# Optimization experiments

Hardware: AMD Instinct MI355X
Metric: run time of the kernel (lower is better)

The kernel has to match this reference:

```python
import math
import jax, jax.numpy as jnp
import numpy as np


def setup_inputs() -> dict:
    key = jax.random.key(0)
    ks = jax.random.split(key, 6)
    b, k, t, h = 4, 128, 2048, 8
    s = 0.05
    return {
        "x": jax.random.normal(ks[0], (b, k, t), dtype=jnp.float32),
        "Wq": jax.random.normal(ks[1], (h * k, k), dtype=jnp.float32) * s,
        "Wk": jax.random.normal(ks[2], (h * k, k), dtype=jnp.float32) * s,
        "Wv": jax.random.normal(ks[3], (h * k, k), dtype=jnp.float32) * s,
        "Wu": jax.random.normal(ks[4], (k, h * k), dtype=jnp.float32) * s,
        "bu": jax.random.normal(ks[5], (k,), dtype=jnp.float32) * s,
    }


def reference(x, Wq, Wk, Wv, Wu, bu):
    b, k, t = x.shape
    h = Wq.shape[0] // k

    def proj(W):
        # x: [b,k,t], W: [h*k, k] -> [b,h,k,t]
        return jnp.einsum('bkt,jk->bjt', x, W).reshape(b, h, k, t)

    q = proj(Wq)
    keys = proj(Wk)
    v = proj(Wv)

    # scores: [b,h,t,t], scaled by 1/sqrt(k)
    dot = jnp.einsum('bhkt,bhki->bhti', q, keys) / math.sqrt(k)
    attn = jax.nn.softmax(dot, axis=-1)

    # attend: [b,h,k,t]
    o = jnp.einsum('bhti,bhki->bhkt', attn, v)

    # unify heads: Wu [k, h*k] viewed as [k,h,k]
    Wu3 = Wu.reshape(k, h, k)
    out = jnp.einsum('bhet,khe->bkt', o, Wu3)
    return out + bu[None, :, None]
```

## Files before the change

kernel.cpp:

```cpp
#include <hip/hip_runtime.h>
#include <hip/hip_bf16.h>

using short8 = __attribute__((ext_vector_type(8))) short;
using f32x4  = __attribute__((ext_vector_type(4))) float;
using f32x16 = __attribute__((ext_vector_type(16))) float;
using uint2v = __attribute__((ext_vector_type(2))) unsigned;

#define B_  4
#define KD  128
#define T_  2048
#define H_  8
#define HK  (H_*KD)
#define NT  (T_/64)

__device__ __forceinline__ ushort f2bf(float f) {
    unsigned u = __builtin_bit_cast(unsigned, f);
    u += 0x7fffu + ((u >> 16) & 1u);
    return (ushort)(u >> 16);
}

__device__ __forceinline__ unsigned cvt_pk_bf16(float lo, float hi) {
    unsigned r;
    asm("v_cvt_pk_bf16_f32 %0, %1, %2" : "=v"(r) : "v"(lo), "v"(hi));
    return r;
}

__global__ __launch_bounds__(256) void prep_kernel(const float* __restrict__ x,
                                                   const float* __restrict__ Wq,
                                                   const float* __restrict__ Wk,
                                                   const float* __restrict__ Wv,
                                                   const float* __restrict__ Wu,
                                                   ushort* __restrict__ wdst,
                                                   ushort* __restrict__ xt) {
    __shared__ float tile[64][65];
    int bx = blockIdx.x;
    if (bx < 2048) {
        int i = bx * 256 + threadIdx.x;
        const int n1 = HK * KD;
        const float* src = (i < n1) ? Wq : (i < 2*n1) ? Wk : (i < 3*n1) ? Wv : Wu;
        wdst[i] = f2bf(src[i & (n1 - 1)]);
        return;
    }
    int bi = bx - 2048;
    int t0 = (bi & 31) * 64;
    int k0 = ((bi >> 5) & 1) * 64;
    int b  = bi >> 6;
    int c  = threadIdx.x & 63;
    int r4 = threadIdx.x >> 6;
    #pragma unroll
    for (int i = 0; i < 16; i++) {
        int k = r4 * 16 + i;
        tile[k][c] = x[((size_t)b * KD + k0 + k) * T_ + t0 + c];
    }
    __syncthreads();
    #pragma unroll
    for (int i = 0; i < 16; i++) {
        int t = r4 * 16 + i;
        xt[((size_t)b * T_ + t0 + t) * KD + k0 + c] = f2bf(tile[c][t]);
    }
}

__global__ __launch_bounds__(256, 2) void proj_kernel(const ushort* __restrict__ xt,
                                                      const ushort* __restrict__ wall,
                                                      ushort* __restrict__ qtb,
                                                      ushort* __restrict__ ktb,
                                                      ushort* __restrict__ vsb) {
    int bz = blockIdx.y;
    int which = bz >> 2, b = bz & 3;
    int tidb = blockIdx.x;
    const ushort *A, *Bp;
    ushort* C;
    int N, m0, n0;
    float scale = 1.f;
    if (which < 2) {
        m0 = (tidb >> 3) * 128;
        n0 = (tidb & 7) * 128;
        A  = xt + (size_t)b * T_ * KD;
        Bp = wall + (size_t)which * (HK * KD);
        C  = (which ? ktb : qtb) + (size_t)b * T_ * HK;
        N  = HK;
        if (which == 0) scale = 0.08838834764831845f;
    } else {
        m0 = (tidb >> 4) * 128;
        n0 = (tidb & 15) * 128;
        A  = wall + (size_t)2 * (HK * KD);
        Bp = xt + (size_t)b * T_ * KD;
        C  = vsb + (size_t)b * HK * T_;
        N  = T_;
    }
    int lane = threadIdx.x & 63;
    int w    = threadIdx.x >> 6;
    int lq = lane & 31, hi = lane >> 5, hi8 = hi * 8;
    m0 += (w >> 1) * 64;
    n0 += (w & 1) * 64;

    const ushort* a0p = A  + (size_t)(m0 + lq) * KD + hi8;
    const ushort* a1p = A  + (size_t)(m0 + 32 + lq) * KD + hi8;
    const ushort* b0p = Bp + (size_t)(n0 + lq) * KD + hi8;
    const ushort* b1p = Bp + (size_t)(n0 + 32 + lq) * KD + hi8;

    short8 a0[8], a1[8], b0[8], b1[8];
    #pragma unroll
    for (int kc = 0; kc < 8; kc++) {
        a0[kc] = *(const short8*)(a0p + kc * 16);
        a1[kc] = *(const short8*)(a1p + kc * 16);
        b0[kc] = *(const short8*)(b0p + kc * 16);
        b1[kc] = *(const short8*)(b1p + kc * 16);
    }
    f32x16 acc[2][2] = {};
    #pragma unroll
    for (int kc = 0; kc < 8; kc++) {
        acc[0][0] = __builtin_amdgcn_mfma_f32_32x32x16_bf16(a0[kc], b0[kc], acc[0][0], 0, 0, 0);
        acc[0][1] = __builtin_amdgcn_mfma_f32_32x32x16_bf16(a0[kc], b1[kc], acc[0][1], 0, 0, 0);
        acc[1][0] = __builtin_amdgcn_mfma_f32_32x32x16_bf16(a1[kc], b0[kc], acc[1][0], 0, 0, 0);
        acc[1][1] = __builtin_amdgcn_mfma_f32_32x32x16_bf16(a1[kc], b1[kc], acc[1][1], 0, 0, 0);
    }
    #pragma unroll
    for (int i = 0; i < 2; i++)
        #pragma unroll
        for (int j = 0; j < 2; j++)
            #pragma unroll
            for (int r = 0; r < 16; r++) {
                int m = m0 + i*32 + (r & 3) + 8 * (r >> 2) + 4 * hi;
                int n = n0 + j*32 + lq;
                C[(size_t)m * N + n] = f2bf(acc[i][j][r] * scale);
            }
}

__global__ __launch_bounds__(256) void gemm_abT_f32bias(const ushort* __restrict__ A,
                                                        const ushort* __restrict__ B, long sB,
                                                        const float* __restrict__ bias,
                                                        float* __restrict__ C, long sC,
                                                        int M, int N, int Kd) {
    int b = blockIdx.z;
    B += (long)b * sB;  C += (long)b * sC;
    int lane = threadIdx.x & 63;
    int w    = threadIdx.x >> 6;
    int lr = lane & 15, lg = lane >> 4;
    int m0 = blockIdx.x * 64 + (w >> 1) * 32;
    int n0 = blockIdx.y * 64 + (w & 1) * 32;

    f32x4 acc[2][2] = {};
    #pragma unroll 4
    for (int k0 = 0; k0 < Kd; k0 += 32) {
        short8 af[2], bf[2];
        #pragma unroll
        for (int i = 0; i < 2; i++)
            af[i] = *(const short8*)(A + (long)(m0 + i*16 + lr) * Kd + k0 + lg*8);
        #pragma unroll
        for (int j = 0; j < 2; j++)
            bf[j] = *(const short8*)(B + (long)(n0 + j*16 + lr) * Kd + k0 + lg*8);
        #pragma unroll
        for (int i = 0; i < 2; i++)
            #pragma unroll
            for (int j = 0; j < 2; j++)
                acc[i][j] = __builtin_amdgcn_mfma_f32_16x16x32_bf16(af[i], bf[j], acc[i][j], 0, 0, 0);
    }
    #pragma unroll
    for (int i = 0; i < 2; i++)
        #pragma unroll
        for (int j = 0; j < 2; j++)
            #pragma unroll
            for (int r = 0; r < 4; r++) {
                int m = m0 + i*16 + lg*4 + r;
                int n = n0 + j*16 + lr;
                C[(long)m * N + n] = acc[i][j][r] + bias[m];
            }
}

__global__ __launch_bounds__(512, 2) void attn32_kernel(const ushort* __restrict__ qt,
                                                        const ushort* __restrict__ kt,
                                                        const ushort* __restrict__ vs,
                                                        ushort* __restrict__ ot) {
    int f = blockIdx.x;
    int xcd = f & 7, u = f >> 3;
    int qt8 = u & 7, gh = u >> 3;
    int g = xcd + 8 * gh;
    int h = g & 7, b = g >> 3;
    int w    = threadIdx.x >> 6;
    int lane = threadIdx.x & 63;
    int lq = lane & 31, hi = lane >> 5;
    int hi8 = hi * 8;
    int q0w = qt8 * 256 + w * 32;

    __shared__ __align__(16) ushort k_lds[2][64 * 128];
    __shared__ __align__(16) ushort v_lds[2][128 * 64];

    int tid  = threadIdx.x;
    int krow = tid >> 3, kcol = (tid & 7) << 4;
    const ushort* kst = kt + ((size_t)b * T_ + krow) * HK + h * KD + kcol;
    int kwi = krow * 128 + (kcol ^ ((krow & 7) << 3));
    int vrow = tid >> 2, vcol = (tid & 3) << 4;
    const ushort* vst = vs + ((size_t)b * HK + h * KD + vrow) * T_ + vcol;
    int vwi = vrow * 64 + (vcol ^ ((vrow & 7) << 3));

    const ushort* qbase = qt + ((size_t)b * T_ + q0w + lq) * HK + h * KD + hi8;

    short8 qf[8];
    #pragma unroll
    for (int dc = 0; dc < 8; dc++)
        qf[dc] = *(const short8*)(qbase + dc * 16);

    short8 rk0 = *(const short8*)(kst);
    short8 rk1 = *(const short8*)(kst + 8);
    short8 rv0 = *(const short8*)(vst);
    short8 rv1 = *(const short8*)(vst + 8);
    *(short8*)&k_lds[0][kwi]     = rk0;
    *(short8*)&k_lds[0][kwi ^ 8] = rk1;
    *(short8*)&v_lds[0][vwi]     = rv0;
    *(short8*)&v_lds[0][vwi ^ 8] = rv1;
    rk0 = *(const short8*)(kst + (size_t)64 * HK);
    rk1 = *(const short8*)(kst + (size_t)64 * HK + 8);
    rv0 = *(const short8*)(vst + 64);
    rv1 = *(const short8*)(vst + 64 + 8);
    __syncthreads();

    f32x16 o_acc[4] = {};
    float m_q = -1e30f, l_q = 0.f;
    const int xsw = (lq & 7) << 3;

    for (int t = 0; t < NT; ++t) {
        const int cur = t & 1;
        f32x16 s0 = {}, s1 = {};
        const ushort* kr0 = &k_lds[cur][(size_t)lq * 128];
        const ushort* kr1 = &k_lds[cur][(size_t)(32 + lq) * 128];
        #pragma unroll
        for (int dc = 0; dc < 8; dc++) {
            int c = (dc * 16 + hi8) ^ xsw;
            short8 kf0 = *(const short8*)(kr0 + c);
            short8 kf1 = *(const short8*)(kr1 + c);
            s0 = __builtin_amdgcn_mfma_f32_32x32x16_bf16(kf0, qf[dc], s0, 0, 0, 0);
            s1 = __builtin_amdgcn_mfma_f32_32x32x16_bf16(kf1, qf[dc], s1, 0, 0, 0);
        }

        float mx[8];
        #pragma unroll
        for (int i = 0; i < 8; i++)
            mx[i] = fmaxf(fmaxf(s0[i], s0[i+8]), fmaxf(s1[i], s1[i+8]));
        #pragma unroll
        for (int st = 4; st > 0; st >>= 1)
            #pragma unroll
            for (int i = 0; i < st; i++) mx[i] = fmaxf(mx[i], mx[i+st]);
        float pmax = fmaxf(mx[0], __shfl_xor(mx[0], 32));

        if (!__all(pmax - m_q <= 8.f)) {
            float mnew = fmaxf(m_q, pmax);
            float corr = __expf(m_q - mnew);
            l_q *= corr;
            m_q = mnew;
            #pragma unroll
            for (int r = 0; r < 16; r++) {
                float cr = __shfl(corr, (r & 3) + 8 * (r >> 2) + 4 * hi);
                #pragma unroll
                for (int dn = 0; dn < 4; dn++) o_acc[dn][r] *= cr;
            }
        }

        float ls0 = 0.f, ls1 = 0.f, ls2 = 0.f, ls3 = 0.f;
        #pragma unroll
        for (int r = 0; r < 16; r++) {
            float e0 = __expf(s0[r] - m_q);
            float e1 = __expf(s1[r] - m_q);
            s0[r] = e0; s1[r] = e1;
            if (r & 1) { ls1 += e0; ls3 += e1; } else { ls0 += e0; ls2 += e1; }
        }
        float lsum = (ls0 + ls1) + (ls2 + ls3);
        lsum += __shfl_xor(lsum, 32);
        l_q += lsum;

        unsigned uu[2][4][2];
        #pragma unroll
        for (int m4 = 0; m4 < 4; m4++) {
            uu[0][m4][0] = cvt_pk_bf16(s0[4*m4+0], s0[4*m4+1]);
            uu[0][m4][1] = cvt_pk_bf16(s0[4*m4+2], s0[4*m4+3]);
            uu[1][m4][0] = cvt_pk_bf16(s1[4*m4+0], s1[4*m4+1]);
            uu[1][m4][1] = cvt_pk_bf16(s1[4*m4+2], s1[4*m4+3]);
        }
        short8 ap[4];
        #pragma unroll
        for (int ks = 0; ks < 4; ks++) {
            int nt = ks >> 1, j = ks & 1;
            unsigned lo0 = uu[nt][2*j][0],   lo1 = uu[nt][2*j][1];
            unsigned hi0 = uu[nt][2*j+1][0], hi1 = uu[nt][2*j+1][1];
            uint2v r0 = __builtin_amdgcn_permlane32_swap(lo0, hi0, false, false);
            uint2v r1 = __builtin_amdgcn_permlane32_swap(lo1, hi1, false, false);
            union { unsigned wd[4]; short8 v; } c;
            c.wd[0] = r0[0];
            c.wd[1] = r1[0];
            c.wd[2] = r0[1];
            c.wd[3] = r1[1];
            ap[ks] = c.v;
        }

        #pragma unroll
        for (int dn = 0; dn < 4; dn++) {
            const ushort* vr = &v_lds[cur][(size_t)(dn*32 + lq) * 64];
            #pragma unroll
            for (int ks = 0; ks < 4; ks++) {
                int c = (ks * 16 + hi8) ^ xsw;
                short8 vf = *(const short8*)(vr + c);
                o_acc[dn] = __builtin_amdgcn_mfma_f32_32x32x16_bf16(ap[ks], vf, o_acc[dn], 0, 0, 0);
            }
        }

        __syncthreads();
        if (t + 1 < NT) {
            const int nxt = cur ^ 1;
            *(short8*)&k_lds[nxt][kwi]     = rk0;
            *(short8*)&k_lds[nxt][kwi ^ 8] = rk1;
            *(short8*)&v_lds[nxt][vwi]     = rv0;
            *(short8*)&v_lds[nxt][vwi ^ 8] = rv1;
            if (t + 2 < NT) {
                size_t ko = (size_t)(t + 2) * 64 * HK;
                int    vo = (t + 2) * 64;
                rk0 = *(const short8*)(kst + ko);
                rk1 = *(const short8*)(kst + ko + 8);
                rv0 = *(const short8*)(vst + vo);
                rv1 = *(const short8*)(vst + vo + 8);
            }
            __syncthreads();
        }
    }

    float linv = 1.f / l_q;
    ushort* ob = ot + ((size_t)b * T_ + q0w) * HK + h * KD;
    #pragma unroll
    for (int r = 0; r < 16; r++) {
        int qrow = (r & 3) + 8 * (r >> 2) + 4 * hi;
        float lr_ = __shfl(linv, qrow);
        #pragma unroll
        for (int dn = 0; dn < 4; dn++)
            ob[(size_t)qrow * HK + dn*32 + lq] = f2bf(o_acc[dn][r] * lr_);
    }
}

extern "C" void kernel_launch(void* const* d_in, const int* in_sizes, int n_in,
                              void* d_out, int out_size, void* d_ws, size_t ws_size,
                              hipStream_t stream) {
    const float* x  = (const float*)d_in[0];
    const float* Wq = (const float*)d_in[1];
    const float* Wk = (const float*)d_in[2];
    const float* Wv = (const float*)d_in[3];
    const float* Wu = (const float*)d_in[4];
    const float* bu = (const float*)d_in[5];
    float* out = (float*)d_out;

    const size_t XT  = (size_t)B_ * T_ * KD * 2;
    const size_t WB  = (size_t)HK * KD * 2;
    const size_t BIG = (size_t)B_ * T_ * HK * 2;
    size_t need = XT + 4*WB + 4*BIG;
    if (ws_size < need) return;

    char* p = (char*)d_ws;
    ushort* xt  = (ushort*)p;            p += XT;
    ushort* wqb = (ushort*)p;            p += WB;
    ushort* wkb = (ushort*)p;            p += WB;
    ushort* wvb = (ushort*)p;            p += WB;
    ushort* wub = (ushort*)p;            p += WB;
    ushort* qtb = (ushort*)p;            p += BIG;
    ushort* ktb = (ushort*)p;            p += BIG;
    ushort* vsb = (ushort*)p;            p += BIG;
    ushort* otb = (ushort*)p;            p += BIG;
    (void)wkb; (void)wvb;

    prep_kernel<<<2304, 256, 0, stream>>>(x, Wq, Wk, Wv, Wu, wqb, xt);

    proj_kernel<<<dim3(128, 12), 256, 0, stream>>>(xt, wqb, qtb, ktb, vsb);

    attn32_kernel<<<dim3(256), 512, 0, stream>>>(qtb, ktb, vsb, otb);

    gemm_abT_f32bias<<<dim3(KD/64, T_/64, B_), 256, 0, stream>>>(
        wub, otb, (long)T_*HK, bu, out, (long)KD*T_, KD, T_, HK);
}
```

Before: 129.7 us.

## Use FP8 for V and probabilities in attention PV matmul

Stores the V projection as FP8 (e4m3) and converts softmax probabilities to FP8, so the PV product runs on the fp8 32x32x16 MFMA and V global and LDS traffic is halved. The V LDS tile is re-laid out with a padded row stride and a new XOR swizzle. The online-softmax rescale threshold is also lowered from 8 to 5, which keeps unnormalized probabilities small enough for the FP8 range but triggers rescales more often. This cuts precision of P and V and risks accuracy loss. The V stores in the projection kernel become scattered byte writes.

```diff
diff --git a/kernel.cpp b/kernel.cpp
--- a/kernel.cpp
+++ b/kernel.cpp
@@ -12,6 +12,7 @@
 #define H_  8
 #define HK  (H_*KD)
 #define NT  (T_/64)
+#define VROW 72
 
 __device__ __forceinline__ ushort f2bf(float f) {
     unsigned u = __builtin_bit_cast(unsigned, f);
@@ -22,6 +23,17 @@
 __device__ __forceinline__ unsigned cvt_pk_bf16(float lo, float hi) {
     unsigned r;
     asm("v_cvt_pk_bf16_f32 %0, %1, %2" : "=v"(r) : "v"(lo), "v"(hi));
+    return r;
+}
+
+__device__ __forceinline__ unsigned cvt_pk_fp8_lo(unsigned old, float a, float b) {
+    unsigned r = old;
+    asm("v_cvt_pk_fp8_f32 %0, %1, %2" : "+v"(r) : "v"(a), "v"(b));
+    return r;
+}
+__device__ __forceinline__ unsigned cvt_pk_fp8_hi(unsigned old, float a, float b) {
+    unsigned r = old;
+    asm("v_cvt_pk_fp8_f32 %0, %1, %2 op_sel:[0,0,1]" : "+v"(r) : "v"(a), "v"(b));
     return r;
 }
 
@@ -64,12 +76,12 @@
                                                       const ushort* __restrict__ wall,
                                                       ushort* __restrict__ qtb,
                                                       ushort* __restrict__ ktb,
-                                                      ushort* __restrict__ vsb) {
+                                                      unsigned char* __restrict__ vsb) {
     int bz = blockIdx.y;
     int which = bz >> 2, b = bz & 3;
     int tidb = blockIdx.x;
     const ushort *A, *Bp;
-    ushort* C;
+    void* Cv;
     int N, m0, n0;
     float scale = 1.f;
     if (which < 2) {
@@ -77,7 +89,7 @@
         n0 = (tidb & 7) * 128;
         A  = xt + (size_t)b * T_ * KD;
         Bp = wall + (size_t)which * (HK * KD);
-        C  = (which ? ktb : qtb) + (size_t)b * T_ * HK;
+        Cv = (which ? ktb : qtb) + (size_t)b * T_ * HK;
         N  = HK;
         if (which == 0) scale = 0.08838834764831845f;
     } else {
@@ -85,7 +97,7 @@
         n0 = (tidb & 15) * 128;
         A  = wall + (size_t)2 * (HK * KD);
         Bp = xt + (size_t)b * T_ * KD;
-        C  = vsb + (size_t)b * HK * T_;
+        Cv = vsb + (size_t)b * HK * T_;
         N  = T_;
     }
     int lane = threadIdx.x & 63;
@@ -115,16 +127,32 @@
         acc[1][0] = __builtin_amdgcn_mfma_f32_32x32x16_bf16(a1[kc], b0[kc], acc[1][0], 0, 0, 0);
         acc[1][1] = __builtin_amdgcn_mfma_f32_32x32x16_bf16(a1[kc], b1[kc], acc[1][1], 0, 0, 0);
     }
-    #pragma unroll
-    for (int i = 0; i < 2; i++)
-        #pragma unroll
-        for (int j = 0; j < 2; j++)
-            #pragma unroll
-            for (int r = 0; r < 16; r++) {
-                int m = m0 + i*32 + (r & 3) + 8 * (r >> 2) + 4 * hi;
-                int n = n0 + j*32 + lq;
-                C[(size_t)m * N + n] = f2bf(acc[i][j][r] * scale);
-            }
+    if (which < 2) {
+        ushort* C = (ushort*)Cv;
+        #pragma unroll
+        for (int i = 0; i < 2; i++)
+            #pragma unroll
+            for (int j = 0; j < 2; j++)
+                #pragma unroll
+                for (int r = 0; r < 16; r++) {
+                    int m = m0 + i*32 + (r & 3) + 8 * (r >> 2) + 4 * hi;
+                    int n = n0 + j*32 + lq;
+                    C[(size_t)m * N + n] = f2bf(acc[i][j][r] * scale);
+                }
+    } else {
+        unsigned char* C = (unsigned char*)Cv;
+        #pragma unroll
+        for (int i = 0; i < 2; i++)
+            #pragma unroll
+            for (int j = 0; j < 2; j++)
+                #pragma unroll
+                for (int r = 0; r < 16; r++) {
+                    int m = m0 + i*32 + (r & 3) + 8 * (r >> 2) + 4 * hi;
+                    int n = n0 + j*32 + lq;
+                    float v = acc[i][j][r];
+                    C[(size_t)m * N + n] = (unsigned char)(cvt_pk_fp8_lo(0u, v, v) & 0xffu);
+                }
+    }
 }
 
 __global__ __launch_bounds__(256) void gemm_abT_f32bias(const ushort* __restrict__ A,
@@ -170,7 +198,7 @@
 
 __global__ __launch_bounds__(512, 2) void attn32_kernel(const ushort* __restrict__ qt,
                                                         const ushort* __restrict__ kt,
-                                                        const ushort* __restrict__ vs,
+                                                        const unsigned char* __restrict__ vs,
                                                         ushort* __restrict__ ot) {
     int f = blockIdx.x;
     int xcd = f & 7, u = f >> 3;
@@ -184,15 +212,15 @@
     int q0w = qt8 * 256 + w * 32;
 
     __shared__ __align__(16) ushort k_lds[2][64 * 128];
-    __shared__ __align__(16) ushort v_lds[2][128 * 64];
+    __shared__ __align__(16) unsigned char v_lds[2][128 * VROW];
 
     int tid  = threadIdx.x;
     int krow = tid >> 3, kcol = (tid & 7) << 4;
     const ushort* kst = kt + ((size_t)b * T_ + krow) * HK + h * KD + kcol;
     int kwi = krow * 128 + (kcol ^ ((krow & 7) << 3));
-    int vrow = tid >> 2, vcol = (tid & 3) << 4;
-    const ushort* vst = vs + ((size_t)b * HK + h * KD + vrow) * T_ + vcol;
-    int vwi = vrow * 64 + (vcol ^ ((vrow & 7) << 3));
+    int vrow = tid >> 2, vc16 = (tid & 3) << 4;
+    const unsigned char* vst = vs + ((size_t)b * HK + h * KD + vrow) * T_ + vc16;
+    int vwb = vrow * VROW + ((((vc16 >> 4) ^ (vrow & 3))) << 4);
 
     const ushort* qbase = qt + ((size_t)b * T_ + q0w + lq) * HK + h * KD + hi8;
 
@@ -203,21 +231,22 @@
 
     short8 rk0 = *(const short8*)(kst);
     short8 rk1 = *(const short8*)(kst + 8);
-    short8 rv0 = *(const short8*)(vst);
-    short8 rv1 = *(const short8*)(vst + 8);
+    long rvlo = *(const long*)(vst);
+    long rvhi = *(const long*)(vst + 8);
     *(short8*)&k_lds[0][kwi]     = rk0;
     *(short8*)&k_lds[0][kwi ^ 8] = rk1;
-    *(short8*)&v_lds[0][vwi]     = rv0;
-    *(short8*)&v_lds[0][vwi ^ 8] = rv1;
+    *(long*)&v_lds[0][vwb]       = rvlo;
+    *(long*)&v_lds[0][vwb + 8]   = rvhi;
     rk0 = *(const short8*)(kst + (size_t)64 * HK);
     rk1 = *(const short8*)(kst + (size_t)64 * HK + 8);
-    rv0 = *(const short8*)(vst + 64);
-    rv1 = *(const short8*)(vst + 64 + 8);
+    rvlo = *(const long*)(vst + 64);
+    rvhi = *(const long*)(vst + 64 + 8);
     __syncthreads();
 
     f32x16 o_acc[4] = {};
     float m_q = -1e30f, l_q = 0.f;
     const int xsw = (lq & 7) << 3;
+    const int vsw = lq & 3;
 
     for (int t = 0; t < NT; ++t) {
         const int cur = t & 1;
@@ -243,7 +272,7 @@
             for (int i = 0; i < st; i++) mx[i] = fmaxf(mx[i], mx[i+st]);
         float pmax = fmaxf(mx[0], __shfl_xor(mx[0], 32));
 
-        if (!__all(pmax - m_q <= 8.f)) {
+        if (!__all(pmax - m_q <= 5.f)) {
             float mnew = fmaxf(m_q, pmax);
             float corr = __expf(m_q - mnew);
             l_q *= corr;
@@ -268,38 +297,26 @@
         lsum += __shfl_xor(lsum, 32);
         l_q += lsum;
 
-        unsigned uu[2][4][2];
-        #pragma unroll
-        for (int m4 = 0; m4 < 4; m4++) {
-            uu[0][m4][0] = cvt_pk_bf16(s0[4*m4+0], s0[4*m4+1]);
-            uu[0][m4][1] = cvt_pk_bf16(s0[4*m4+2], s0[4*m4+3]);
-            uu[1][m4][0] = cvt_pk_bf16(s1[4*m4+0], s1[4*m4+1]);
-            uu[1][m4][1] = cvt_pk_bf16(s1[4*m4+2], s1[4*m4+3]);
-        }
-        short8 ap[4];
+        long ap8[4];
         #pragma unroll
         for (int ks = 0; ks < 4; ks++) {
-            int nt = ks >> 1, j = ks & 1;
-            unsigned lo0 = uu[nt][2*j][0],   lo1 = uu[nt][2*j][1];
-            unsigned hi0 = uu[nt][2*j+1][0], hi1 = uu[nt][2*j+1][1];
-            uint2v r0 = __builtin_amdgcn_permlane32_swap(lo0, hi0, false, false);
-            uint2v r1 = __builtin_amdgcn_permlane32_swap(lo1, hi1, false, false);
-            union { unsigned wd[4]; short8 v; } c;
-            c.wd[0] = r0[0];
-            c.wd[1] = r1[0];
-            c.wd[2] = r0[1];
-            c.wd[3] = r1[1];
-            ap[ks] = c.v;
+            const f32x16& sN = (ks < 2) ? s0 : s1;
+            int rb = (ks & 1) * 8;
+            unsigned F0 = cvt_pk_fp8_lo(0u, sN[rb+0], sN[rb+1]);
+            F0 = cvt_pk_fp8_hi(F0, sN[rb+2], sN[rb+3]);
+            unsigned F1 = cvt_pk_fp8_lo(0u, sN[rb+4], sN[rb+5]);
+            F1 = cvt_pk_fp8_hi(F1, sN[rb+6], sN[rb+7]);
+            uint2v d01 = __builtin_amdgcn_permlane32_swap(F0, F1, false, false);
+            ap8[ks] = (long)(((unsigned long)d01[1] << 32) | (unsigned long)d01[0]);
         }
 
         #pragma unroll
         for (int dn = 0; dn < 4; dn++) {
-            const ushort* vr = &v_lds[cur][(size_t)(dn*32 + lq) * 64];
+            const unsigned char* vr = &v_lds[cur][(size_t)(dn*32 + lq) * VROW];
             #pragma unroll
             for (int ks = 0; ks < 4; ks++) {
-                int c = (ks * 16 + hi8) ^ xsw;
-                short8 vf = *(const short8*)(vr + c);
-                o_acc[dn] = __builtin_amdgcn_mfma_f32_32x32x16_bf16(ap[ks], vf, o_acc[dn], 0, 0, 0);
+                long vf = *(const long*)(vr + ((ks ^ vsw) << 4) + hi8);
+                o_acc[dn] = __builtin_amdgcn_mfma_f32_32x32x16_fp8_fp8(ap8[ks], vf, o_acc[dn], 0, 0, 0);
             }
         }
 
@@ -308,15 +325,15 @@
             const int nxt = cur ^ 1;
             *(short8*)&k_lds[nxt][kwi]     = rk0;
             *(short8*)&k_lds[nxt][kwi ^ 8] = rk1;
-            *(short8*)&v_lds[nxt][vwi]     = rv0;
-            *(short8*)&v_lds[nxt][vwi ^ 8] = rv1;
+            *(long*)&v_lds[nxt][vwb]       = rvlo;
+            *(long*)&v_lds[nxt][vwb + 8]   = rvhi;
             if (t + 2 < NT) {
                 size_t ko = (size_t)(t + 2) * 64 * HK;
                 int    vo = (t + 2) * 64;
                 rk0 = *(const short8*)(kst + ko);
                 rk1 = *(const short8*)(kst + ko + 8);
-                rv0 = *(const short8*)(vst + vo);
-                rv1 = *(const short8*)(vst + vo + 8);
+                rvlo = *(const long*)(vst + vo);
+                rvhi = *(const long*)(vst + vo + 8);
             }
             __syncthreads();
         }
@@ -348,7 +365,8 @@
     const size_t XT  = (size_t)B_ * T_ * KD * 2;
     const size_t WB  = (size_t)HK * KD * 2;
     const size_t BIG = (size_t)B_ * T_ * HK * 2;
-    size_t need = XT + 4*WB + 4*BIG;
+    const size_t VSZ = (size_t)B_ * HK * T_;
+    size_t need = XT + 4*WB + 3*BIG + VSZ;
     if (ws_size < need) return;
 
     char* p = (char*)d_ws;
@@ -359,7 +377,7 @@
     ushort* wub = (ushort*)p;            p += WB;
     ushort* qtb = (ushort*)p;            p += BIG;
     ushort* ktb = (ushort*)p;            p += BIG;
-    ushort* vsb = (ushort*)p;            p += BIG;
+    unsigned char* vsb = (unsigned char*)p;  p += VSZ;
     ushort* otb = (ushort*)p;            p += BIG;
     (void)wkb; (void)wvb;
 
```

Result: faster. 122.8 us (-5.3%).
